# Kernel tuning notes

Hardware: AMD Instinct MI355X
Metric: run time of the kernel (lower is better)

## Reference

```python
import jax, jax.numpy as jnp
import numpy as np

B, N, D, H, M, NN, K = 2, 2048, 256, 8, 2, 2048, 8


def setup_inputs() -> dict:
    key = jax.random.key(0)
    ks = jax.random.split(key, 8)
    s = 0.02
    return {
        "current_points": jax.random.normal(ks[0], (B, N, 3), jnp.float32),
        "current_features": jax.random.normal(ks[1], (B, N, D), jnp.float32),
        "neighbor_points": jax.random.normal(ks[2], (M, B, NN, 3), jnp.float32),
        "neighbor_features": jax.random.normal(ks[3], (M, B, NN, D), jnp.float32),
        "in_proj_w": jax.random.normal(ks[4], (3 * D, D), jnp.float32) * s,
        "in_proj_b": jnp.zeros((3 * D,), jnp.float32),
        "out_proj_w": jax.random.normal(ks[5], (D, D), jnp.float32) * s,
        "out_proj_b": jnp.zeros((D,), jnp.float32),
        "spatial_w": jax.random.normal(ks[6], (D, 3), jnp.float32) * s,
        "spatial_b": jnp.zeros((D,), jnp.float32),
    }


def _knn_edge_features(points, features, k):
    # points [b,n,3], features [b,n,d] -> edge features [b,n,d]
    sq = jnp.sum(points * points, axis=-1)                       # [b,n]
    d2 = sq[:, :, None] + sq[:, None, :] - 2.0 * jnp.einsum('bnc,bmc->bnm', points, points)
    _, idx = jax.lax.top_k(-d2, k)                               # k nearest (incl. self), [b,n,k]
    b_idx = jnp.arange(points.shape[0])[:, None, None]
    nbr = features[b_idx, idx]                                   # gather neighbor feats [b,n,k,d]
    return features - jnp.mean(nbr, axis=2)


def _mha(q, kv, in_w, in_b, out_w, out_b, h):
    # torch nn.MultiheadAttention (batch_first) cross-attention
    d = q.shape[-1]
    dh = d // h
    wq, wk, wv = jnp.split(in_w, 3, axis=0)
    bq, bk, bv = jnp.split(in_b, 3, axis=0)
    qp = q @ wq.T + bq                                           # [b,Lq,d]
    kp = kv @ wk.T + bk                                          # [b,Lk,d]
    vp = kv @ wv.T + bv

    def heads(x):
        b, l, _ = x.shape
        return x.reshape(b, l, h, dh).transpose(0, 2, 1, 3)      # [b,h,l,dh]

    qh, kh, vh = heads(qp), heads(kp), heads(vp)
    scores = jnp.einsum('bhqd,bhkd->bhqk', qh, kh) / np.sqrt(dh).astype(np.float32)
    attn = jax.nn.softmax(scores, axis=-1)
    o = jnp.einsum('bhqk,bhkd->bhqd', attn, vh)
    b, _, lq, _ = o.shape
    o = o.transpose(0, 2, 1, 3).reshape(b, lq, d)
    return o @ out_w.T + out_b


def reference(current_points, current_features, neighbor_points, neighbor_features,
              in_proj_w, in_proj_b, out_proj_w, out_proj_b, spatial_w, spatial_b):
    cur_edge = _knn_edge_features(current_points, current_features, K)       # [B,N,D]
    nbr_edge = jax.vmap(lambda p, f: _knn_edge_features(p, f, K))(neighbor_points, neighbor_features)  # [M,B,NN,D]
    all_nbr = jnp.transpose(nbr_edge, (1, 0, 2, 3)).reshape(B, M * NN, D)    # cat along seq dim
    aligned = _mha(cur_edge, all_nbr, in_proj_w, in_proj_b, out_proj_w, out_proj_b, H)
    spatial = current_points @ spatial_w.T + spatial_b                       # [B,N,D]
    return aligned + spatial
```

## Files before the change

kernel.cpp:

```cpp
#include <hip/hip_runtime.h>
#include <hip/hip_bf16.h>

typedef __bf16 bf16_t;
typedef __attribute__((ext_vector_type(8))) __bf16 bf16x8;
typedef __attribute__((ext_vector_type(4))) __bf16 bf16x4;
typedef __attribute__((ext_vector_type(4))) float f32x4;


__global__ __launch_bounds__(256) void wconv_kernel(const float* __restrict__ w_in,
                                                    const float* __restrict__ w_out,
                                                    bf16_t* __restrict__ w_in_b,
                                                    bf16_t* __restrict__ w_out_b) {
    int i = blockIdx.x * 256 + threadIdx.x;
    if (i < 768 * 256) w_in_b[i] = (bf16_t)w_in[i];
    if (i < 256 * 256) w_out_b[i] = (bf16_t)w_out[i];
}

__global__ __launch_bounds__(1024) void knn_kernel(const float* __restrict__ cur_pts,
                                                   const float* __restrict__ nbr_pts,
                                                   int* __restrict__ idx_out) {
    int p = blockIdx.y;
    const float* pts = (p < 2) ? (cur_pts + (size_t)p * 2048 * 3)
                               : (nbr_pts + (size_t)(p - 2) * 2048 * 3);

    __shared__ __align__(16) float4 spts[2048];

    int tid = threadIdx.x;
    for (int i = tid; i < 2048; i += 1024) {
        float x = pts[i * 3 + 0], y = pts[i * 3 + 1], z = pts[i * 3 + 2];
        float sq = __fadd_rn(__fadd_rn(__fmul_rn(x, x), __fmul_rn(y, y)), __fmul_rn(z, z));
        spts[i] = make_float4(x, y, z, sq);
    }
    __syncthreads();

    int wave = tid >> 6, lane = tid & 63;
    int q = blockIdx.x * 16 + wave;
    float4 qp4 = spts[q];

    float dist[8];
    int di[8];
#pragma unroll
    for (int r = 0; r < 8; r++) { dist[r] = 3.4e38f; di[r] = 0x7fffffff; }

    for (int t = 0; t < 32; t++) {
        int j = t * 64 + lane;
        float4 pp = spts[j];
        float dot = __fadd_rn(__fadd_rn(__fmul_rn(qp4.x, pp.x), __fmul_rn(qp4.y, pp.y)),
                              __fmul_rn(qp4.z, pp.z));
        float d2 = __fsub_rn(__fadd_rn(qp4.w, pp.w), __fmul_rn(2.0f, dot));
        if (d2 < dist[7]) {
#pragma unroll
            for (int r = 7; r >= 1; --r) {
                bool cm = d2 < dist[r - 1];
                bool cr = d2 < dist[r];
                float nd = cm ? dist[r - 1] : (cr ? d2 : dist[r]);
                int ni = cm ? di[r - 1] : (cr ? j : di[r]);
                dist[r] = nd; di[r] = ni;
            }
            if (d2 < dist[0]) { dist[0] = d2; di[0] = j; }
        }
    }

    int res[8];
#pragma unroll
    for (int r = 0; r < 8; r++) {
        float bd = dist[0];
        int bi = di[0];
#pragma unroll
        for (int m = 1; m < 64; m <<= 1) {
            float od = __shfl_xor(bd, m);
            int oi = __shfl_xor(bi, m);
            if (od < bd || (od == bd && oi < bi)) { bd = od; bi = oi; }
        }
        res[r] = bi;
        bool win = (di[0] == bi);
#pragma unroll
        for (int k = 0; k < 7; k++) {
            dist[k] = win ? dist[k + 1] : dist[k];
            di[k]   = win ? di[k + 1]   : di[k];
        }
        if (win) { dist[7] = 3.4e38f; di[7] = 0x7fffffff; }
    }

    if (lane == 0) {
        int4* o = (int4*)(idx_out + ((size_t)p * 2048 + q) * 8);
        o[0] = make_int4(res[0], res[1], res[2], res[3]);
        o[1] = make_int4(res[4], res[5], res[6], res[7]);
    }
}

__global__ __launch_bounds__(64) void edge_kernel(const float* __restrict__ cur_feat,
                                                  const float* __restrict__ nbr_feat,
                                                  const int* __restrict__ idx_buf,
                                                  bf16_t* __restrict__ cur_edge,
                                                  bf16_t* __restrict__ all_nbr) {
    int blk = blockIdx.x;
    int p = blk >> 11, q = blk & 2047;
    const float* feat;
    bf16_t* outp;
    if (p < 2) {
        feat = cur_feat + (size_t)p * 2048 * 256;
        outp = cur_edge + ((size_t)p * 2048 + q) * 256;
    } else {
        int mb = p - 2;
        int m = mb >> 1, bb = mb & 1;
        feat = nbr_feat + (size_t)mb * 2048 * 256;
        outp = all_nbr + ((size_t)bb * 4096 + m * 2048 + q) * 256;
    }
    const int* idx = idx_buf + ((size_t)p * 2048 + q) * 8;
    int t = threadIdx.x;
    float4 self = ((const float4*)(feat + (size_t)q * 256))[t];
    float sx = 0.f, sy = 0.f, sz = 0.f, sw = 0.f;
#pragma unroll
    for (int r = 0; r < 8; r++) {
        float4 f = ((const float4*)(feat + (size_t)idx[r] * 256))[t];
        sx += f.x; sy += f.y; sz += f.z; sw += f.w;
    }
    bf16x4 v;
    v[0] = (bf16_t)(self.x - sx * 0.125f);
    v[1] = (bf16_t)(self.y - sy * 0.125f);
    v[2] = (bf16_t)(self.z - sz * 0.125f);
    v[3] = (bf16_t)(self.w - sw * 0.125f);
    *(bf16x4*)(outp + 4 * t) = v;
}

__global__ __launch_bounds__(256) void qkv_kernel(const bf16_t* __restrict__ cur_edge,
                                                  const bf16_t* __restrict__ all_nbr,
                                                  const bf16_t* __restrict__ w_in,
                                                  const float* __restrict__ b_in,
                                                  bf16_t* __restrict__ qp,
                                                  bf16_t* __restrict__ kp,
                                                  bf16_t* __restrict__ vpT) {
    int z = blockIdx.z;
    int Mrows = (z == 0) ? 4096 : 8192;
    int m0base = blockIdx.y * 64;
    if (m0base >= Mrows) return;
    const bf16_t* A = (z == 0) ? cur_edge : all_nbr;
    const bf16_t* W = w_in + (size_t)z * 256 * 256;

    int wave = threadIdx.x >> 6, lane = threadIdx.x & 63;
    int wr = wave >> 1, wc = wave & 1;
    int m0 = m0base + wr * 32;
    int n0 = blockIdx.x * 64 + wc * 32;
    int lr = lane & 15, lg = lane >> 4;

    f32x4 acc[2][2] = {};
    for (int kc = 0; kc < 256; kc += 32) {
        bf16x8 a[2], b[2];
#pragma unroll
        for (int i = 0; i < 2; i++)
            a[i] = *(const bf16x8*)(A + (size_t)(m0 + i * 16 + lr) * 256 + kc + lg * 8);
#pragma unroll
        for (int i = 0; i < 2; i++)
            b[i] = *(const bf16x8*)(W + (size_t)(n0 + i * 16 + lr) * 256 + kc + lg * 8);
#pragma unroll
        for (int i = 0; i < 2; i++)
#pragma unroll
            for (int j = 0; j < 2; j++)
                acc[i][j] = __builtin_amdgcn_mfma_f32_16x16x32_bf16(a[i], b[j], acc[i][j], 0, 0, 0);
    }

    const float inv_s = 0.17677669529663687f;
#pragma unroll
    for (int i = 0; i < 2; i++)
#pragma unroll
        for (int j = 0; j < 2; j++)
#pragma unroll
            for (int r = 0; r < 4; r++) {
                int mm = m0 + i * 16 + lg * 4 + r;
                int nn = n0 + j * 16 + lr;
                float v = acc[i][j][r] + b_in[z * 256 + nn];
                if (z == 0) {
                    qp[(size_t)mm * 256 + nn] = (bf16_t)(v * inv_s);
                } else if (z == 1) {
                    kp[(size_t)mm * 256 + nn] = (bf16_t)v;
                } else {
                    int bb = mm >> 12, kv = mm & 4095, h = nn >> 5, dd = nn & 31;
                    vpT[(((size_t)bb * 8 + h) * 32 + dd) * 4096 + kv] = (bf16_t)v;
                }
            }
}

__global__ __launch_bounds__(256, 8) void attn_kernel(const bf16_t* __restrict__ qp,
                                                      const bf16_t* __restrict__ kp,
                                                      const bf16_t* __restrict__ vpT,
                                                      bf16_t* __restrict__ Opart,
                                                      float* __restrict__ Lpart) {
    int bh = blockIdx.y;
    int b = bh >> 3, h = bh & 7;
    int c = blockIdx.z;
    int wave = threadIdx.x >> 6, lane = threadIdx.x & 63;
    int lr = lane & 15, lg = lane >> 4;
    int q0 = blockIdx.x * 64 + wave * 16;

    const bf16_t* Qb = qp + ((size_t)b * 2048 + q0) * 256 + h * 32;
    const bf16_t* Kb = kp + (size_t)b * 4096 * 256 + h * 32;
    const bf16_t* Vb = vpT + ((size_t)b * 8 + h) * 32 * 4096;

    __shared__ __align__(16) bf16_t KV[2048];
    __shared__ __align__(16) bf16_t P_lds[4][512];
    bf16_t* Pw = &P_lds[wave][0];

    bf16x8 qfrag = *(const bf16x8*)(Qb + (size_t)lr * 256 + lg * 8);

    f32x4 oacc[2] = {};
    float lsum[4] = {};
    const f32x4 zf = {0.f, 0.f, 0.f, 0.f};

    int kv_lo = c * 1024;

    int role = wave;
    int tlr = lr, tlg = lg;
    const bf16_t* gsrc;
    size_t gstep;
    if (role < 2) {
        gsrc = Kb + (size_t)(kv_lo + role * 16 + tlr) * 256 + tlg * 8;
        gstep = 32 * 256;
    } else {
        gsrc = Vb + (size_t)((role - 2) * 16 + tlr) * 4096 + kv_lo + tlg * 8;
        gstep = 32;
    }
    bf16_t* stage_dst = &KV[(size_t)threadIdx.x * 8];

    bf16x8 g = *(const bf16x8*)gsrc;
    gsrc += gstep;

    for (int t = 0; t < 32; t++) {
        *(bf16x8*)stage_dst = g;
        if (t + 1 < 32) {
            g = *(const bf16x8*)gsrc;
            gsrc += gstep;
        }
        __syncthreads();

        bf16x8 kf0 = *(const bf16x8*)(KV + (size_t)lane * 8);
        bf16x8 kf1 = *(const bf16x8*)(KV + 512 + (size_t)lane * 8);
        bf16x8 vf0 = *(const bf16x8*)(KV + 1024 + (size_t)lane * 8);
        bf16x8 vf1 = *(const bf16x8*)(KV + 1536 + (size_t)lane * 8);

        f32x4 s0 = __builtin_amdgcn_mfma_f32_16x16x32_bf16(qfrag, kf0, zf, 0, 0, 0);
        f32x4 s1 = __builtin_amdgcn_mfma_f32_16x16x32_bf16(qfrag, kf1, zf, 0, 0, 0);
#pragma unroll
        for (int r = 0; r < 4; r++) {
            float p0 = __expf(s0[r]);
            float p1 = __expf(s1[r]);
            lsum[r] += p0 + p1;
            Pw[((lr >> 3) * 128) + (lg * 4 + r) * 8 + (lr & 7)] = (bf16_t)p0;
            Pw[((2 + (lr >> 3)) * 128) + (lg * 4 + r) * 8 + (lr & 7)] = (bf16_t)p1;
        }
        bf16x8 pf = *(const bf16x8*)(Pw + (size_t)lane * 8);
        oacc[0] = __builtin_amdgcn_mfma_f32_16x16x32_bf16(pf, vf0, oacc[0], 0, 0, 0);
        oacc[1] = __builtin_amdgcn_mfma_f32_16x16x32_bf16(pf, vf1, oacc[1], 0, 0, 0);

        __syncthreads();
    }

#pragma unroll
    for (int r = 0; r < 4; r++) {
        float s = lsum[r];
        s += __shfl_xor(s, 1);
        s += __shfl_xor(s, 2);
        s += __shfl_xor(s, 4);
        s += __shfl_xor(s, 8);
        lsum[r] = s;
    }

#pragma unroll
    for (int r = 0; r < 4; r++) {
        int qq = q0 + lg * 4 + r;
        if (lr == 0)
            Lpart[(((size_t)c * 2 + b) * 8 + h) * 2048 + qq] = lsum[r];
#pragma unroll
        for (int ds = 0; ds < 2; ds++) {
            int dd = h * 32 + ds * 16 + lr;
            Opart[(((size_t)c * 2 + b) * 2048 + qq) * 256 + dd] = (bf16_t)oacc[ds][r];
        }
    }
}

__global__ __launch_bounds__(256) void attn_combine(const bf16_t* __restrict__ Opart,
                                                    const float* __restrict__ Lpart,
                                                    bf16_t* __restrict__ o_buf) {
    int t = blockIdx.x * 256 + threadIdx.x;
    int row = t >> 5;
    int c8 = (t & 31) * 8;
    int b = row >> 11, q = row & 2047, h = c8 >> 5;

    float acc[8] = {};
    float l = 0.f;
#pragma unroll
    for (int c = 0; c < 4; c++) {
        bf16x8 v = *(const bf16x8*)(Opart + (((size_t)c * 2 + b) * 2048 + q) * 256 + c8);
#pragma unroll
        for (int j = 0; j < 8; j++) acc[j] += (float)v[j];
        l += Lpart[(((size_t)c * 2 + b) * 8 + h) * 2048 + q];
    }
    float rl = 1.0f / l;
    bf16x8 o;
#pragma unroll
    for (int j = 0; j < 8; j++) o[j] = (bf16_t)(acc[j] * rl);
    *(bf16x8*)(o_buf + (size_t)row * 256 + c8) = o;
}

__global__ __launch_bounds__(256) void outproj_kernel(const bf16_t* __restrict__ o_buf,
                                                      const bf16_t* __restrict__ w_out,
                                                      const float* __restrict__ b_out,
                                                      const float* __restrict__ cur_pts,
                                                      const float* __restrict__ sw,
                                                      const float* __restrict__ sb,
                                                      float* __restrict__ out) {
    int wave = threadIdx.x >> 6, lane = threadIdx.x & 63;
    int wr = wave >> 1, wc = wave & 1;
    int m0 = blockIdx.y * 64 + wr * 32;
    int n0 = blockIdx.x * 64 + wc * 32;
    int lr = lane & 15, lg = lane >> 4;

    f32x4 acc[2][2] = {};
    for (int kc = 0; kc < 256; kc += 32) {
        bf16x8 a[2], b[2];
#pragma unroll
        for (int i = 0; i < 2; i++)
            a[i] = *(const bf16x8*)(o_buf + (size_t)(m0 + i * 16 + lr) * 256 + kc + lg * 8);
#pragma unroll
        for (int i = 0; i < 2; i++)
            b[i] = *(const bf16x8*)(w_out + (size_t)(n0 + i * 16 + lr) * 256 + kc + lg * 8);
#pragma unroll
        for (int i = 0; i < 2; i++)
#pragma unroll
            for (int j = 0; j < 2; j++)
                acc[i][j] = __builtin_amdgcn_mfma_f32_16x16x32_bf16(a[i], b[j], acc[i][j], 0, 0, 0);
    }

#pragma unroll
    for (int i = 0; i < 2; i++)
#pragma unroll
        for (int j = 0; j < 2; j++)
#pragma unroll
            for (int r = 0; r < 4; r++) {
                int mm = m0 + i * 16 + lg * 4 + r;
                int nn = n0 + j * 16 + lr;
                const float* pp = cur_pts + (size_t)mm * 3;
                float sp = pp[0] * sw[nn * 3 + 0] + pp[1] * sw[nn * 3 + 1] + pp[2] * sw[nn * 3 + 2] + sb[nn];
                out[(size_t)mm * 256 + nn] = acc[i][j][r] + b_out[nn] + sp;
            }
}

extern "C" void kernel_launch(void* const* d_in, const int* in_sizes, int n_in,
                              void* d_out, int out_size, void* d_ws, size_t ws_size,
                              hipStream_t stream) {
    const float* cur_pts  = (const float*)d_in[0];
    const float* cur_feat = (const float*)d_in[1];
    const float* nbr_pts  = (const float*)d_in[2];
    const float* nbr_feat = (const float*)d_in[3];
    const float* in_w     = (const float*)d_in[4];
    const float* in_b     = (const float*)d_in[5];
    const float* out_w    = (const float*)d_in[6];
    const float* out_b    = (const float*)d_in[7];
    const float* sw       = (const float*)d_in[8];
    const float* sb       = (const float*)d_in[9];

    char* ws = (char*)d_ws;
    bf16_t* w_in_b  = (bf16_t*)(ws + 0);
    bf16_t* w_out_b = (bf16_t*)(ws + 393216);
    int*    idx_buf = (int*)(ws + 524288);
    bf16_t* cur_edge = (bf16_t*)(ws + 917504);
    bf16_t* all_nbr  = (bf16_t*)(ws + 3014656);
    bf16_t* qp  = (bf16_t*)(ws + 7208960);
    bf16_t* kp  = (bf16_t*)(ws + 9306112);
    bf16_t* vpT = (bf16_t*)(ws + 13500416);
    bf16_t* o_buf = (bf16_t*)(ws + 17694720);
    bf16_t* Opart = (bf16_t*)(ws + 19791872);
    float*  Lpart = (float*)(ws + 28180480);
    float* outp = (float*)d_out;

    wconv_kernel<<<dim3(768), dim3(256), 0, stream>>>(in_w, out_w, w_in_b, w_out_b);
    knn_kernel<<<dim3(128, 6), dim3(1024), 0, stream>>>(cur_pts, nbr_pts, idx_buf);
    edge_kernel<<<dim3(12288), dim3(64), 0, stream>>>(cur_feat, nbr_feat, idx_buf, cur_edge, all_nbr);
    qkv_kernel<<<dim3(4, 128, 3), dim3(256), 0, stream>>>(cur_edge, all_nbr, w_in_b, in_b, qp, kp, vpT);
    attn_kernel<<<dim3(32, 16, 4), dim3(256), 0, stream>>>(qp, kp, vpT, Opart, Lpart);
    attn_combine<<<dim3(512), dim3(256), 0, stream>>>(Opart, Lpart, o_buf);
    outproj_kernel<<<dim3(4, 64), dim3(256), 0, stream>>>(o_buf, w_out_b, out_b, cur_pts, sw, sb, outp);
}
```

Baseline: 202.6 us.

## Double-buffer K/V staging in attention and remap blocks for XCD locality

The attention kernel now stages K/V tiles into two LDS buffers with a two-tile-deep register prefetch, so only one barrier per tile is needed instead of two, and the next global load overlaps compute. The launch grid is flattened to 1D and the block index is remapped so that blocks sharing the same (batch, head, chunk) land on the same XCD, which should improve L2 reuse of K/V. It adds extra registers and LDS use, manual sched_barriers and waitcnt asm, and more intricate loop logic.

New measurement: 202.5 us. No clear change (-0.1%).

```diff
diff --git a/kernel.cpp b/kernel.cpp
--- a/kernel.cpp
+++ b/kernel.cpp
@@ -186,18 +186,23 @@
                                                       const bf16_t* __restrict__ vpT,
                                                       bf16_t* __restrict__ Opart,
                                                       float* __restrict__ Lpart) {
-    int bh = blockIdx.y;
+    int d = blockIdx.x;
+    int xcd = d & 7;
+    int j = d >> 3;
+    int xb = j & 31;
+    int g = xcd + 8 * (j >> 5);
+    int bh = g & 15, c = g >> 4;
     int b = bh >> 3, h = bh & 7;
-    int c = blockIdx.z;
+
     int wave = threadIdx.x >> 6, lane = threadIdx.x & 63;
     int lr = lane & 15, lg = lane >> 4;
-    int q0 = blockIdx.x * 64 + wave * 16;
+    int q0 = xb * 64 + wave * 16;
 
     const bf16_t* Qb = qp + ((size_t)b * 2048 + q0) * 256 + h * 32;
     const bf16_t* Kb = kp + (size_t)b * 4096 * 256 + h * 32;
     const bf16_t* Vb = vpT + ((size_t)b * 8 + h) * 32 * 4096;
 
-    __shared__ __align__(16) bf16_t KV[2048];
+    __shared__ __align__(16) bf16_t KV[2][2048];
     __shared__ __align__(16) bf16_t P_lds[4][512];
     bf16_t* Pw = &P_lds[wave][0];
 
@@ -209,51 +214,69 @@
 
     int kv_lo = c * 1024;
 
-    int role = wave;
-    int tlr = lr, tlg = lg;
     const bf16_t* gsrc;
     size_t gstep;
-    if (role < 2) {
-        gsrc = Kb + (size_t)(kv_lo + role * 16 + tlr) * 256 + tlg * 8;
+    if (wave < 2) {
+        gsrc = Kb + (size_t)(kv_lo + wave * 16 + lr) * 256 + lg * 8;
         gstep = 32 * 256;
     } else {
-        gsrc = Vb + (size_t)((role - 2) * 16 + tlr) * 4096 + kv_lo + tlg * 8;
+        gsrc = Vb + (size_t)((wave - 2) * 16 + lr) * 4096 + kv_lo + lg * 8;
         gstep = 32;
     }
-    bf16_t* stage_dst = &KV[(size_t)threadIdx.x * 8];
-
-    bf16x8 g = *(const bf16x8*)gsrc;
-    gsrc += gstep;
-
-    for (int t = 0; t < 32; t++) {
-        *(bf16x8*)stage_dst = g;
-        if (t + 1 < 32) {
-            g = *(const bf16x8*)gsrc;
-            gsrc += gstep;
+    const int sdst = threadIdx.x * 8;
+
+#define BARRIER()                                          \
+    asm volatile("s_waitcnt lgkmcnt(0)" ::: "memory");     \
+    __builtin_amdgcn_sched_barrier(0);                     \
+    __builtin_amdgcn_s_barrier();                          \
+    __builtin_amdgcn_sched_barrier(0);
+
+#define COMPUTE(BUF)                                                           \
+    {                                                                          \
+        bf16x8 kf0 = *(const bf16x8*)(&KV[BUF][0] + (size_t)lane * 8);         \
+        bf16x8 kf1 = *(const bf16x8*)(&KV[BUF][512] + (size_t)lane * 8);       \
+        bf16x8 vf0 = *(const bf16x8*)(&KV[BUF][1024] + (size_t)lane * 8);      \
+        bf16x8 vf1 = *(const bf16x8*)(&KV[BUF][1536] + (size_t)lane * 8);      \
+        f32x4 s0 = __builtin_amdgcn_mfma_f32_16x16x32_bf16(qfrag, kf0, zf, 0, 0, 0); \
+        f32x4 s1 = __builtin_amdgcn_mfma_f32_16x16x32_bf16(qfrag, kf1, zf, 0, 0, 0); \
+        _Pragma("unroll")                                                      \
+        for (int r = 0; r < 4; r++) {                                          \
+            float p0 = __expf(s0[r]);                                          \
+            float p1 = __expf(s1[r]);                                          \
+            lsum[r] += p0 + p1;                                                \
+            Pw[((lr >> 3) * 128) + (lg * 4 + r) * 8 + (lr & 7)] = (bf16_t)p0;  \
+            Pw[((2 + (lr >> 3)) * 128) + (lg * 4 + r) * 8 + (lr & 7)] = (bf16_t)p1; \
+        }                                                                      \
+        bf16x8 pf = *(const bf16x8*)(Pw + (size_t)lane * 8);                   \
+        oacc[0] = __builtin_amdgcn_mfma_f32_16x16x32_bf16(pf, vf0, oacc[0], 0, 0, 0); \
+        oacc[1] = __builtin_amdgcn_mfma_f32_16x16x32_bf16(pf, vf1, oacc[1], 0, 0, 0); \
+    }
+
+    bf16x8 g0 = *(const bf16x8*)gsrc; gsrc += gstep;
+    bf16x8 gA = *(const bf16x8*)gsrc; gsrc += gstep;
+    bf16x8 gB = *(const bf16x8*)gsrc; gsrc += gstep;
+    *(bf16x8*)(&KV[0][0] + sdst) = g0;
+    BARRIER()
+
+#pragma unroll 1
+    for (int i = 0; i < 16; i++) {
+        bf16x8 gA2, gB2;
+        if (i < 15) { gA2 = *(const bf16x8*)gsrc; gsrc += gstep; }
+        __builtin_amdgcn_sched_barrier(0);
+        COMPUTE(0)
+        *(bf16x8*)(&KV[1][0] + sdst) = gA;
+        BARRIER()
+        if (i < 14) { gB2 = *(const bf16x8*)gsrc; gsrc += gstep; }
+        __builtin_amdgcn_sched_barrier(0);
+        COMPUTE(1)
+        if (i < 15) {
+            *(bf16x8*)(&KV[0][0] + sdst) = gB;
+            BARRIER()
         }
-        __syncthreads();
-
-        bf16x8 kf0 = *(const bf16x8*)(KV + (size_t)lane * 8);
-        bf16x8 kf1 = *(const bf16x8*)(KV + 512 + (size_t)lane * 8);
-        bf16x8 vf0 = *(const bf16x8*)(KV + 1024 + (size_t)lane * 8);
-        bf16x8 vf1 = *(const bf16x8*)(KV + 1536 + (size_t)lane * 8);
-
-        f32x4 s0 = __builtin_amdgcn_mfma_f32_16x16x32_bf16(qfrag, kf0, zf, 0, 0, 0);
-        f32x4 s1 = __builtin_amdgcn_mfma_f32_16x16x32_bf16(qfrag, kf1, zf, 0, 0, 0);
-#pragma unroll
-        for (int r = 0; r < 4; r++) {
-            float p0 = __expf(s0[r]);
-            float p1 = __expf(s1[r]);
-            lsum[r] += p0 + p1;
-            Pw[((lr >> 3) * 128) + (lg * 4 + r) * 8 + (lr & 7)] = (bf16_t)p0;
-            Pw[((2 + (lr >> 3)) * 128) + (lg * 4 + r) * 8 + (lr & 7)] = (bf16_t)p1;
-        }
-        bf16x8 pf = *(const bf16x8*)(Pw + (size_t)lane * 8);
-        oacc[0] = __builtin_amdgcn_mfma_f32_16x16x32_bf16(pf, vf0, oacc[0], 0, 0, 0);
-        oacc[1] = __builtin_amdgcn_mfma_f32_16x16x32_bf16(pf, vf1, oacc[1], 0, 0, 0);
-
-        __syncthreads();
-    }
+        gA = gA2; gB = gB2;
+    }
+#undef COMPUTE
+#undef BARRIER
 
 #pragma unroll
     for (int r = 0; r < 4; r++) {
@@ -377,7 +400,7 @@
     knn_kernel<<<dim3(128, 6), dim3(1024), 0, stream>>>(cur_pts, nbr_pts, idx_buf);
     edge_kernel<<<dim3(12288), dim3(64), 0, stream>>>(cur_feat, nbr_feat, idx_buf, cur_edge, all_nbr);
     qkv_kernel<<<dim3(4, 128, 3), dim3(256), 0, stream>>>(cur_edge, all_nbr, w_in_b, in_b, qp, kp, vpT);
-    attn_kernel<<<dim3(32, 16, 4), dim3(256), 0, stream>>>(qp, kp, vpT, Opart, Lpart);
+    attn_kernel<<<dim3(2048), dim3(256), 0, stream>>>(qp, kp, vpT, Opart, Lpart);
     attn_combine<<<dim3(512), dim3(256), 0, stream>>>(Opart, Lpart, o_buf);
     outproj_kernel<<<dim3(4, 64), dim3(256), 0, stream>>>(o_buf, w_out_b, out_b, cur_pts, sw, sb, outp);
 }
```
